# Performance work log

Measured on AMD Instinct MI355X. Metric: run time of the kernel, lower is better.

Reference implementation:

```python
import jax, jax.numpy as jnp
import numpy as np
import math

B, S, D, H = 2, 2048, 1024, 16
DK = D // H


def setup_inputs() -> dict:
    key = jax.random.key(0)
    ks = jax.random.split(key, 14)
    inp = {
        "query": jax.random.normal(ks[0], (B, S, D), dtype=jnp.float32),
        "key": jax.random.normal(ks[1], (B, S, D), dtype=jnp.float32),
        "value": jax.random.normal(ks[2], (B, S, D), dtype=jnp.float32),
        "group_prob": jax.random.uniform(ks[3], (B, S, S), dtype=jnp.float32),
        "mask": jax.random.randint(ks[4], (B, S), 0, 2, dtype=jnp.int32),
    }
    scale = 0.02
    inp["Wq"] = jax.random.normal(ks[5], (D, D), dtype=jnp.float32) * scale
    inp["bq"] = jnp.zeros((D,), dtype=jnp.float32)
    inp["Wk"] = jax.random.normal(ks[6], (D, D), dtype=jnp.float32) * scale
    inp["bk"] = jnp.zeros((D,), dtype=jnp.float32)
    inp["Wv"] = jax.random.normal(ks[7], (D, D), dtype=jnp.float32) * scale
    inp["bv"] = jnp.zeros((D,), dtype=jnp.float32)
    inp["Wo"] = jax.random.normal(ks[8], (D, D), dtype=jnp.float32) * scale
    inp["bo"] = jnp.zeros((D,), dtype=jnp.float32)
    return inp


def reference(query, key, value, group_prob, mask, Wq, bq, Wk, bk, Wv, bv, Wo, bo):
    b, s, d = query.shape
    # project and split heads: [B,S,D] -> [B,H,S,DK]
    def proj(x, W, bias):
        return (x @ W.T + bias).reshape(b, s, H, DK).transpose(0, 2, 1, 3)

    q = proj(query, Wq, bq)
    k = proj(key, Wk, bk)
    v = proj(value, Wv, bv)

    scores = jnp.einsum("bhqd,bhkd->bhqk", q, k) / math.sqrt(DK)  # [B,H,S,S]

    # combined mask: padding-row mask OR diagonal (always attend to self)
    eye = jnp.eye(s, dtype=jnp.int32)
    combined = mask[:, None, None, :] | eye[None, None, :, :]  # [B,1,S,S]
    scores = jnp.where(combined == 0, jnp.float32(-1e9), scores)

    p_attn = jax.nn.softmax(scores, axis=-1)
    p_attn = p_attn * group_prob[:, None, :, :]  # post-softmax group scaling

    x = jnp.einsum("bhqk,bhkd->bhqd", p_attn, v)  # [B,H,S,DK]
    x = x.transpose(0, 2, 1, 3).reshape(b, s, d)
    return x @ Wo.T + bo
```

## Files before the change

### kernel.cpp

```cpp
#include <hip/hip_runtime.h>
#include <hip/hip_bf16.h>
#include <stdint.h>

typedef __bf16 bf16x8 __attribute__((ext_vector_type(8)));
typedef float f32x4 __attribute__((ext_vector_type(4)));

#define QSCALE 0.1803368801111244f

__device__ __forceinline__ void gld16(const void* g, void* l) {
  __builtin_amdgcn_global_load_lds(
      (__attribute__((address_space(1))) void*)(uintptr_t)(g),
      (__attribute__((address_space(3))) void*)(l), 16, 0, 0);
}

struct CastArgs {
  const float* src[7];
  __bf16* dst[7];
  int n[7];
};

__global__ __launch_bounds__(256) void cast_bf16_kernel(CastArgs a) {
  const int t = blockIdx.y;
  const int i = (blockIdx.x * 256 + threadIdx.x) * 8;
  if (i >= a.n[t]) return;
  const float4* s = (const float4*)(a.src[t] + i);
  float4 v0 = s[0], v1 = s[1];
  bf16x8 o;
  o[0] = (__bf16)v0.x; o[1] = (__bf16)v0.y; o[2] = (__bf16)v0.z; o[3] = (__bf16)v0.w;
  o[4] = (__bf16)v1.x; o[5] = (__bf16)v1.y; o[6] = (__bf16)v1.z; o[7] = (__bf16)v1.w;
  *(bf16x8*)(a.dst[t] + i) = o;
}

struct QkvArgs {
  const __bf16* A[3];
  const __bf16* B[3];
  const float* bias[3];
  __bf16* out[3];
};

__global__ __launch_bounds__(256) void qkv_gemm(QkvArgs args) {
  __shared__ __align__(16) __bf16 As[128 * 32];
  __shared__ __align__(16) __bf16 Bs[128 * 32];
  const int tid = threadIdx.x;
  const int z = blockIdx.y;
  const int bx = blockIdx.x;
  const int m0 = (z < 2 ? (bx >> 3) : (bx & 7)) * 128;
  const int n0 = (z < 2 ? (bx & 7) : (bx >> 3)) * 128;
  const __bf16* A = args.A[z];
  const __bf16* B = args.B[z];
  const float* bias = args.bias[z];
  __bf16* out = args.out[z];
  const float scale = (z == 0) ? QSCALE : 1.0f;

  const int lane = tid & 63, wid = tid >> 6;
  const int wm = (wid & 1) * 64, wn = (wid >> 1) * 64;
  const int l16 = lane & 15, quad = lane >> 4;

  const int sc = (tid & 3) ^ ((tid >> 2) & 3);
  const __bf16* ga = A + (size_t)(m0 + (tid >> 2)) * 1024 + sc * 8;
  const __bf16* gb = B + (size_t)(n0 + (tid >> 2)) * 1024 + sc * 8;
  char* lA = (char*)As + tid * 16;
  char* lB = (char*)Bs + tid * 16;
  const int a_off = (wm + l16) * 64 + ((quad ^ (l16 & 3)) * 16);
  const int b_off = (wn + l16) * 64 + ((quad ^ (l16 & 3)) * 16);

  f32x4 acc[4][4] = {};

  for (int k0 = 0; k0 < 1024; k0 += 32) {
    __syncthreads();
    gld16(ga + k0, lA);
    gld16(ga + k0 + 64 * 1024, lA + 4096);
    gld16(gb + k0, lB);
    gld16(gb + k0 + 64 * 1024, lB + 4096);
    __syncthreads();
    bf16x8 af[4], bfr[4];
#pragma unroll
    for (int mi = 0; mi < 4; ++mi)
      af[mi] = *(const bf16x8*)((const char*)As + a_off + mi * 1024);
#pragma unroll
    for (int ni = 0; ni < 4; ++ni)
      bfr[ni] = *(const bf16x8*)((const char*)Bs + b_off + ni * 1024);
#pragma unroll
    for (int mi = 0; mi < 4; ++mi)
#pragma unroll
      for (int ni = 0; ni < 4; ++ni)
        acc[mi][ni] = __builtin_amdgcn_mfma_f32_16x16x32_bf16(af[mi], bfr[ni],
                                                              acc[mi][ni], 0, 0, 0);
  }

  if (z < 2) {
#pragma unroll
    for (int ni = 0; ni < 4; ++ni) {
      const int col = n0 + wn + ni * 16 + l16;
      const int h = col >> 6, dk = col & 63;
      const float bb = bias[col];
#pragma unroll
      for (int mi = 0; mi < 4; ++mi)
#pragma unroll
        for (int r = 0; r < 4; ++r) {
          const int row = m0 + wm + mi * 16 + quad * 4 + r;
          const int b = row >> 11, s = row & 2047;
          out[((size_t)(b * 16 + h) * 2048 + s) * 64 + dk] =
              (__bf16)((acc[mi][ni][r] + bb) * scale);
        }
    }
  } else {
#pragma unroll
    for (int mi = 0; mi < 4; ++mi)
#pragma unroll
      for (int r = 0; r < 4; ++r) {
        const int rowm = m0 + wm + mi * 16 + quad * 4 + r;
        const int h = rowm >> 6, dk = rowm & 63;
        const float bb = bias[rowm];
#pragma unroll
        for (int ni = 0; ni < 4; ++ni) {
          const int coln = n0 + wn + ni * 16 + l16;
          const int b = coln >> 11, s = coln & 2047;
          out[((size_t)(b * 16 + h) * 64 + dk) * 2048 + s] =
              (__bf16)(acc[mi][ni][r] + bb);
        }
      }
  }
}

__global__ __launch_bounds__(256) void gemm_out(const __bf16* __restrict__ A,
                                                const __bf16* __restrict__ B,
                                                const float* __restrict__ bias,
                                                float* __restrict__ out) {
  __shared__ __align__(16) __bf16 As[128 * 32];
  __shared__ __align__(16) __bf16 Bs[128 * 32];
  const int tid = threadIdx.x;
  const int m0 = blockIdx.y * 128;
  const int n0 = blockIdx.x * 128;
  const int lane = tid & 63, wid = tid >> 6;
  const int wm = (wid & 1) * 64, wn = (wid >> 1) * 64;
  const int l16 = lane & 15, quad = lane >> 4;

  const int sc = (tid & 3) ^ ((tid >> 2) & 3);
  const __bf16* ga = A + (size_t)(m0 + (tid >> 2)) * 1024 + sc * 8;
  const __bf16* gb = B + (size_t)(n0 + (tid >> 2)) * 1024 + sc * 8;
  char* lA = (char*)As + tid * 16;
  char* lB = (char*)Bs + tid * 16;
  const int a_off = (wm + l16) * 64 + ((quad ^ (l16 & 3)) * 16);
  const int b_off = (wn + l16) * 64 + ((quad ^ (l16 & 3)) * 16);

  f32x4 acc[4][4] = {};

  for (int k0 = 0; k0 < 1024; k0 += 32) {
    __syncthreads();
    gld16(ga + k0, lA);
    gld16(ga + k0 + 64 * 1024, lA + 4096);
    gld16(gb + k0, lB);
    gld16(gb + k0 + 64 * 1024, lB + 4096);
    __syncthreads();
    bf16x8 af[4], bfr[4];
#pragma unroll
    for (int mi = 0; mi < 4; ++mi)
      af[mi] = *(const bf16x8*)((const char*)As + a_off + mi * 1024);
#pragma unroll
    for (int ni = 0; ni < 4; ++ni)
      bfr[ni] = *(const bf16x8*)((const char*)Bs + b_off + ni * 1024);
#pragma unroll
    for (int mi = 0; mi < 4; ++mi)
#pragma unroll
      for (int ni = 0; ni < 4; ++ni)
        acc[mi][ni] = __builtin_amdgcn_mfma_f32_16x16x32_bf16(af[mi], bfr[ni],
                                                              acc[mi][ni], 0, 0, 0);
  }

#pragma unroll
  for (int ni = 0; ni < 4; ++ni) {
    const int col = n0 + wn + ni * 16 + l16;
    const float bb = bias[col];
#pragma unroll
    for (int mi = 0; mi < 4; ++mi)
#pragma unroll
      for (int r = 0; r < 4; ++r) {
        const int row = m0 + wm + mi * 16 + quad * 4 + r;
        out[(size_t)row * 1024 + col] = acc[mi][ni][r] + bb;
      }
  }
}

__global__ __launch_bounds__(512, 4) void attn_kernel(
    const __bf16* __restrict__ Qh, const __bf16* __restrict__ Kh,
    const __bf16* __restrict__ Vt, const float* __restrict__ gprob,
    const int* __restrict__ maskp, __bf16* __restrict__ xb) {
  __shared__ __align__(16) __bf16 Ks[2][64 * 64];
  __shared__ __align__(16) __bf16 Vs[2][64 * 64];
  __shared__ unsigned long long mbits[32];

  const int tid = threadIdx.x;
  const int qt = blockIdx.x, bh = blockIdx.y;
  const int b = bh >> 4, h = bh & 15;
  const int q0 = qt * 128;
  const int lane = tid & 63, wid = tid >> 6, l16 = lane & 15, quad = lane >> 4;
  const size_t head_off = (size_t)bh * (2048 * 64);

  const int srow = tid >> 3;
  const int sc8 = (tid & 7) ^ (srow & 7);
  const int fxor = (l16 & 7);

  const int sig = ((srow & 16) << 1) + ((srow & 12) << 1) + ((srow & 32) >> 3) +
                  (srow & 3);

  const __bf16* gk0 = Kh + head_off + (size_t)sig * 64 + sc8 * 8;
  const __bf16* gv0 = Vt + head_off + (size_t)srow * 2048 + sc8 * 8;

  gld16(gk0, (char*)Ks + tid * 16);
  gld16(gv0, (char*)Vs + tid * 16);

  bf16x8 aq[2];
  {
    const __bf16* gq = Qh + head_off + (size_t)(q0 + wid * 16 + l16) * 64 + quad * 8;
    aq[0] = *(const bf16x8*)(gq);
    aq[1] = *(const bf16x8*)(gq + 32);
  }

  int irow[4];
#pragma unroll
  for (int r = 0; r < 4; ++r) irow[r] = q0 + wid * 16 + quad * 4 + r;

  const float* gpl = gprob + (size_t)b * 2048 * 2048 +
                     (size_t)(q0 + wid * 16 + l16) * 2048 + quad * 8;
  float4 g0 = *(const float4*)(gpl);
  float4 g1 = *(const float4*)(gpl + 4);
  float4 g2 = *(const float4*)(gpl + 32);
  float4 g3 = *(const float4*)(gpl + 36);

  {
    const int* mr = maskp + b * 2048;
#pragma unroll
    for (int t = 0; t < 4; ++t) {
      const int kt2 = wid * 4 + t;
      const int mv = mr[kt2 * 64 + lane];
      const unsigned long long bal = __ballot(mv != 0);
      if (lane == 0) mbits[kt2] = bal;
    }
  }
  __syncthreads();

  f32x4 o[4] = {};
  float lp = 0.f;

  const int dkt = qt * 2 + (wid >> 2);
  const int kqbase = (wid & 3) * 16 + l16 - quad * 8;

  for (int kt = 0; kt < 32; ++kt) {
    const int cur = kt & 1;
    float4 gn0, gn1, gn2, gn3;
    if (kt < 31) {
      const int nb = cur ^ 1;
      gld16(gk0 + (kt + 1) * 4096, (char*)Ks + nb * 8192 + tid * 16);
      gld16(gv0 + (kt + 1) * 64, (char*)Vs + nb * 8192 + tid * 16);
      const float* gn = gpl + (kt + 1) * 64;
      gn0 = *(const float4*)(gn);
      gn1 = *(const float4*)(gn + 4);
      gn2 = *(const float4*)(gn + 32);
      gn3 = *(const float4*)(gn + 36);
    }

    const unsigned long long sh = mbits[kt] >> (quad * 8);
    const uint32_t shlo = (uint32_t)sh, shhi = (uint32_t)(sh >> 32);

    f32x4 p2[4] = {};
#pragma unroll
    for (int kh = 0; kh < 2; ++kh)
#pragma unroll
      for (int ni = 0; ni < 4; ++ni) {
        bf16x8 bk = *(const bf16x8*)((const char*)Ks + cur * 8192 +
                                     (ni * 16 + l16) * 128 +
                                     (((kh * 4 + quad) ^ fxor) * 16));
        p2[ni] = __builtin_amdgcn_mfma_f32_16x16x32_bf16(bk, aq[kh], p2[ni], 0, 0, 0);
      }

    const float gfl[16] = {g0.x, g0.y, g0.z, g0.w, g1.x, g1.y, g1.z, g1.w,
                           g2.x, g2.y, g2.z, g2.w, g3.x, g3.y, g3.z, g3.w};
    bf16x8 pa0, pa1;
    if (kt != dkt) {
#pragma unroll
      for (int ni = 0; ni < 4; ++ni)
#pragma unroll
        for (int r = 0; r < 4; ++r) {
          const int j = ((ni >> 1) << 2) + r;
          const float e = __builtin_exp2f(p2[ni][r]);
          const bool mk = (((ni & 1) ? shhi : shlo) >> j) & 1;
          const float em = mk ? e : 0.f;
          lp += em;
          const float pg = em * gfl[(ni & 1) * 8 + j];
          if (ni & 1) pa1[j] = (__bf16)pg; else pa0[j] = (__bf16)pg;
        }
    } else {
#pragma unroll
      for (int ni = 0; ni < 4; ++ni)
#pragma unroll
        for (int r = 0; r < 4; ++r) {
          const int j = ((ni >> 1) << 2) + r;
          const float e = __builtin_exp2f(p2[ni][r]);
          const bool mk = (((ni & 1) ? shhi : shlo) >> j) & 1;
          const bool diag = (kqbase == ((ni & 1) * 32 + j));
          const float em = (mk || diag) ? e : 0.f;
          lp += em;
          const float pg = em * gfl[(ni & 1) * 8 + j];
          if (ni & 1) pa1[j] = (__bf16)pg; else pa0[j] = (__bf16)pg;
        }
    }

#pragma unroll
    for (int kh = 0; kh < 2; ++kh) {
      const bf16x8 pa = kh ? pa1 : pa0;
#pragma unroll
      for (int ni = 0; ni < 4; ++ni) {
        bf16x8 bv = *(const bf16x8*)((const char*)Vs + cur * 8192 +
                                     (ni * 16 + l16) * 128 +
                                     (((kh * 4 + quad) ^ fxor) * 16));
        o[ni] = __builtin_amdgcn_mfma_f32_16x16x32_bf16(pa, bv, o[ni], 0, 0, 0);
      }
    }

    if (kt < 31) { g0 = gn0; g1 = gn1; g2 = gn2; g3 = gn3; }
    __syncthreads();
  }

  lp += __shfl_xor(lp, 16);
  lp += __shfl_xor(lp, 32);
  float rinv[4];
#pragma unroll
  for (int r = 0; r < 4; ++r) rinv[r] = 1.f / __shfl(lp, quad * 4 + r);
#pragma unroll
  for (int ni = 0; ni < 4; ++ni) {
    const int dk = ni * 16 + l16;
#pragma unroll
    for (int r = 0; r < 4; ++r) {
      const float val = o[ni][r] * rinv[r];
      xb[((size_t)(b * 2048 + irow[r])) * 1024 + h * 64 + dk] = (__bf16)val;
    }
  }
}

extern "C" void kernel_launch(void* const* d_in, const int* in_sizes, int n_in,
                              void* d_out, int out_size, void* d_ws, size_t ws_size,
                              hipStream_t stream) {
  const float* query = (const float*)d_in[0];
  const float* key_  = (const float*)d_in[1];
  const float* value = (const float*)d_in[2];
  const float* gprob = (const float*)d_in[3];
  const int*   maskp = (const int*)d_in[4];
  const float* Wq = (const float*)d_in[5];
  const float* bq = (const float*)d_in[6];
  const float* Wk = (const float*)d_in[7];
  const float* bk = (const float*)d_in[8];
  const float* Wv = (const float*)d_in[9];
  const float* bv = (const float*)d_in[10];
  const float* Wo = (const float*)d_in[11];
  const float* bo = (const float*)d_in[12];

  char* ws = (char*)d_ws;
  const size_t MB = 1 << 20;
  __bf16* qb  = (__bf16*)(ws + 0 * MB);
  __bf16* kb  = (__bf16*)(ws + 8 * MB);
  __bf16* vb  = (__bf16*)(ws + 16 * MB);
  __bf16* Wqb = (__bf16*)(ws + 24 * MB);
  __bf16* Wkb = (__bf16*)(ws + 26 * MB);
  __bf16* Wvb = (__bf16*)(ws + 28 * MB);
  __bf16* Wob = (__bf16*)(ws + 30 * MB);
  __bf16* Qh  = (__bf16*)(ws + 32 * MB);
  __bf16* Kh  = (__bf16*)(ws + 40 * MB);
  __bf16* Vt  = (__bf16*)(ws + 48 * MB);
  __bf16* xb  = (__bf16*)(ws + 56 * MB);

  CastArgs ca;
  ca.src[0] = query; ca.dst[0] = qb;  ca.n[0] = 4194304;
  ca.src[1] = key_;  ca.dst[1] = kb;  ca.n[1] = 4194304;
  ca.src[2] = value; ca.dst[2] = vb;  ca.n[2] = 4194304;
  ca.src[3] = Wq;    ca.dst[3] = Wqb; ca.n[3] = 1048576;
  ca.src[4] = Wk;    ca.dst[4] = Wkb; ca.n[4] = 1048576;
  ca.src[5] = Wv;    ca.dst[5] = Wvb; ca.n[5] = 1048576;
  ca.src[6] = Wo;    ca.dst[6] = Wob; ca.n[6] = 1048576;
  cast_bf16_kernel<<<dim3(2048, 7), 256, 0, stream>>>(ca);

  QkvArgs qa;
  qa.A[0] = qb;  qa.B[0] = Wqb; qa.bias[0] = bq; qa.out[0] = Qh;
  qa.A[1] = kb;  qa.B[1] = Wkb; qa.bias[1] = bk; qa.out[1] = Kh;
  qa.A[2] = Wvb; qa.B[2] = vb;  qa.bias[2] = bv; qa.out[2] = Vt;
  qkv_gemm<<<dim3(256, 3), 256, 0, stream>>>(qa);

  attn_kernel<<<dim3(16, 32), 512, 0, stream>>>(Qh, Kh, Vt, gprob, maskp, xb);
  gemm_out<<<dim3(8, 32), 256, 0, stream>>>(xb, Wob, bo, (float*)d_out);
}
```

Measured before the change: 301.9 us.

## Process two key tiles per iteration and interleave softmax with MFMA under priority

The attention loop now handles two 64-key tiles per iteration with a double-buffered 128-key LDS stage, halving the number of block barriers. The QK MFMAs for both tiles are issued together and the softmax of tile B is scheduled after tile A's PV MFMAs, with s_setprio raised around the MFMA blocks so matrix work and exp/pack work from different waves overlap. Group-probability loads are issued just in time per tile. LDS use doubles (64KB per block), which may reduce occupancy relative to the declared 4 blocks per CU, and register pressure rises.

```diff
diff --git a/kernel.cpp b/kernel.cpp
--- a/kernel.cpp
+++ b/kernel.cpp
@@ -182,12 +182,33 @@
   }
 }
 
+template <bool DIAG>
+__device__ __forceinline__ void smpack(const f32x4 (&p2)[4], uint32_t shlo,
+                                       uint32_t shhi, const float* gfl,
+                                       int kqbase, float& lp, bf16x8& pa0,
+                                       bf16x8& pa1) {
+#pragma unroll
+  for (int ni = 0; ni < 4; ++ni)
+#pragma unroll
+    for (int r = 0; r < 4; ++r) {
+      const int j = ((ni >> 1) << 2) + r;
+      const float e = __builtin_exp2f(p2[ni][r]);
+      const bool mk = (((ni & 1) ? shhi : shlo) >> j) & 1;
+      bool keep = mk;
+      if (DIAG) keep = mk || (kqbase == ((ni & 1) * 32 + j));
+      const float em = keep ? e : 0.f;
+      lp += em;
+      const float pg = em * gfl[(ni & 1) * 8 + j];
+      if (ni & 1) pa1[j] = (__bf16)pg; else pa0[j] = (__bf16)pg;
+    }
+}
+
 __global__ __launch_bounds__(512, 4) void attn_kernel(
     const __bf16* __restrict__ Qh, const __bf16* __restrict__ Kh,
     const __bf16* __restrict__ Vt, const float* __restrict__ gprob,
     const int* __restrict__ maskp, __bf16* __restrict__ xb) {
-  __shared__ __align__(16) __bf16 Ks[2][64 * 64];
-  __shared__ __align__(16) __bf16 Vs[2][64 * 64];
+  __shared__ __align__(16) __bf16 Ks[2][128 * 64];
+  __shared__ __align__(16) __bf16 Vs[2][128 * 64];
   __shared__ unsigned long long mbits[32];
 
   const int tid = threadIdx.x;
@@ -208,7 +229,9 @@
   const __bf16* gv0 = Vt + head_off + (size_t)srow * 2048 + sc8 * 8;
 
   gld16(gk0, (char*)Ks + tid * 16);
+  gld16(gk0 + 4096, (char*)Ks + 8192 + tid * 16);
   gld16(gv0, (char*)Vs + tid * 16);
+  gld16(gv0 + 64, (char*)Vs + 8192 + tid * 16);
 
   bf16x8 aq[2];
   {
@@ -217,16 +240,12 @@
     aq[1] = *(const bf16x8*)(gq + 32);
   }
 
-  int irow[4];
-#pragma unroll
-  for (int r = 0; r < 4; ++r) irow[r] = q0 + wid * 16 + quad * 4 + r;
-
   const float* gpl = gprob + (size_t)b * 2048 * 2048 +
                      (size_t)(q0 + wid * 16 + l16) * 2048 + quad * 8;
-  float4 g0 = *(const float4*)(gpl);
-  float4 g1 = *(const float4*)(gpl + 4);
-  float4 g2 = *(const float4*)(gpl + 32);
-  float4 g3 = *(const float4*)(gpl + 36);
+  float4 gA0 = *(const float4*)(gpl);
+  float4 gA1 = *(const float4*)(gpl + 4);
+  float4 gA2 = *(const float4*)(gpl + 32);
+  float4 gA3 = *(const float4*)(gpl + 36);
 
   {
     const int* mr = maskp + b * 2048;
@@ -246,79 +265,103 @@
   const int dkt = qt * 2 + (wid >> 2);
   const int kqbase = (wid & 3) * 16 + l16 - quad * 8;
 
-  for (int kt = 0; kt < 32; ++kt) {
-    const int cur = kt & 1;
-    float4 gn0, gn1, gn2, gn3;
-    if (kt < 31) {
+  for (int tt = 0; tt < 16; ++tt) {
+    const int cur = tt & 1;
+    const int kkA = 2 * tt, kkB = 2 * tt + 1;
+    if (tt < 15) {
       const int nb = cur ^ 1;
-      gld16(gk0 + (kt + 1) * 4096, (char*)Ks + nb * 8192 + tid * 16);
-      gld16(gv0 + (kt + 1) * 64, (char*)Vs + nb * 8192 + tid * 16);
-      const float* gn = gpl + (kt + 1) * 64;
-      gn0 = *(const float4*)(gn);
-      gn1 = *(const float4*)(gn + 4);
-      gn2 = *(const float4*)(gn + 32);
-      gn3 = *(const float4*)(gn + 36);
-    }
-
-    const unsigned long long sh = mbits[kt] >> (quad * 8);
-    const uint32_t shlo = (uint32_t)sh, shhi = (uint32_t)(sh >> 32);
-
-    f32x4 p2[4] = {};
+      gld16(gk0 + (size_t)(kkA + 2) * 4096, (char*)Ks + nb * 16384 + tid * 16);
+      gld16(gk0 + (size_t)(kkB + 2) * 4096, (char*)Ks + nb * 16384 + 8192 + tid * 16);
+      gld16(gv0 + (kkA + 2) * 64, (char*)Vs + nb * 16384 + tid * 16);
+      gld16(gv0 + (kkB + 2) * 64, (char*)Vs + nb * 16384 + 8192 + tid * 16);
+    }
+    const float* gbp = gpl + (size_t)kkB * 64;
+    float4 gB0 = *(const float4*)(gbp);
+    float4 gB1 = *(const float4*)(gbp + 4);
+    float4 gB2 = *(const float4*)(gbp + 32);
+    float4 gB3 = *(const float4*)(gbp + 36);
+
+    const unsigned long long shA = mbits[kkA] >> (quad * 8);
+    const unsigned long long shB = mbits[kkB] >> (quad * 8);
+
+    f32x4 p2a[4] = {}, p2b[4] = {};
+    const char* ksA = (const char*)Ks + cur * 16384;
+    const char* ksB = ksA + 8192;
+    __builtin_amdgcn_s_setprio(1);
 #pragma unroll
     for (int kh = 0; kh < 2; ++kh)
 #pragma unroll
       for (int ni = 0; ni < 4; ++ni) {
-        bf16x8 bk = *(const bf16x8*)((const char*)Ks + cur * 8192 +
-                                     (ni * 16 + l16) * 128 +
+        bf16x8 bk = *(const bf16x8*)(ksA + (ni * 16 + l16) * 128 +
                                      (((kh * 4 + quad) ^ fxor) * 16));
-        p2[ni] = __builtin_amdgcn_mfma_f32_16x16x32_bf16(bk, aq[kh], p2[ni], 0, 0, 0);
-      }
-
-    const float gfl[16] = {g0.x, g0.y, g0.z, g0.w, g1.x, g1.y, g1.z, g1.w,
-                           g2.x, g2.y, g2.z, g2.w, g3.x, g3.y, g3.z, g3.w};
-    bf16x8 pa0, pa1;
-    if (kt != dkt) {
-#pragma unroll
-      for (int ni = 0; ni < 4; ++ni)
-#pragma unroll
-        for (int r = 0; r < 4; ++r) {
-          const int j = ((ni >> 1) << 2) + r;
-          const float e = __builtin_exp2f(p2[ni][r]);
-          const bool mk = (((ni & 1) ? shhi : shlo) >> j) & 1;
-          const float em = mk ? e : 0.f;
-          lp += em;
-          const float pg = em * gfl[(ni & 1) * 8 + j];
-          if (ni & 1) pa1[j] = (__bf16)pg; else pa0[j] = (__bf16)pg;
-        }
-    } else {
-#pragma unroll
-      for (int ni = 0; ni < 4; ++ni)
-#pragma unroll
-        for (int r = 0; r < 4; ++r) {
-          const int j = ((ni >> 1) << 2) + r;
-          const float e = __builtin_exp2f(p2[ni][r]);
-          const bool mk = (((ni & 1) ? shhi : shlo) >> j) & 1;
-          const bool diag = (kqbase == ((ni & 1) * 32 + j));
-          const float em = (mk || diag) ? e : 0.f;
-          lp += em;
-          const float pg = em * gfl[(ni & 1) * 8 + j];
-          if (ni & 1) pa1[j] = (__bf16)pg; else pa0[j] = (__bf16)pg;
-        }
-    }
-
+        p2a[ni] = __builtin_amdgcn_mfma_f32_16x16x32_bf16(bk, aq[kh], p2a[ni], 0, 0, 0);
+      }
+#pragma unroll
+    for (int kh = 0; kh < 2; ++kh)
+#pragma unroll
+      for (int ni = 0; ni < 4; ++ni) {
+        bf16x8 bk = *(const bf16x8*)(ksB + (ni * 16 + l16) * 128 +
+                                     (((kh * 4 + quad) ^ fxor) * 16));
+        p2b[ni] = __builtin_amdgcn_mfma_f32_16x16x32_bf16(bk, aq[kh], p2b[ni], 0, 0, 0);
+      }
+    __builtin_amdgcn_s_setprio(0);
+
+    bf16x8 paA0, paA1;
+    {
+      const float gfl[16] = {gA0.x, gA0.y, gA0.z, gA0.w, gA1.x, gA1.y, gA1.z, gA1.w,
+                             gA2.x, gA2.y, gA2.z, gA2.w, gA3.x, gA3.y, gA3.z, gA3.w};
+      if (kkA == dkt)
+        smpack<true>(p2a, (uint32_t)shA, (uint32_t)(shA >> 32), gfl, kqbase, lp, paA0, paA1);
+      else
+        smpack<false>(p2a, (uint32_t)shA, (uint32_t)(shA >> 32), gfl, kqbase, lp, paA0, paA1);
+    }
+
+    const char* vsA = (const char*)Vs + cur * 16384;
+    const char* vsB = vsA + 8192;
+    __builtin_amdgcn_s_setprio(1);
 #pragma unroll
     for (int kh = 0; kh < 2; ++kh) {
-      const bf16x8 pa = kh ? pa1 : pa0;
+      const bf16x8 pa = kh ? paA1 : paA0;
 #pragma unroll
       for (int ni = 0; ni < 4; ++ni) {
-        bf16x8 bv = *(const bf16x8*)((const char*)Vs + cur * 8192 +
-                                     (ni * 16 + l16) * 128 +
+        bf16x8 bv = *(const bf16x8*)(vsA + (ni * 16 + l16) * 128 +
                                      (((kh * 4 + quad) ^ fxor) * 16));
         o[ni] = __builtin_amdgcn_mfma_f32_16x16x32_bf16(pa, bv, o[ni], 0, 0, 0);
       }
     }
-
-    if (kt < 31) { g0 = gn0; g1 = gn1; g2 = gn2; g3 = gn3; }
+    __builtin_amdgcn_s_setprio(0);
+
+    if (tt < 15) {
+      const float* gap = gpl + (size_t)(kkA + 2) * 64;
+      gA0 = *(const float4*)(gap);
+      gA1 = *(const float4*)(gap + 4);
+      gA2 = *(const float4*)(gap + 32);
+      gA3 = *(const float4*)(gap + 36);
+    }
+
+    bf16x8 paB0, paB1;
+    {
+      const float gfl[16] = {gB0.x, gB0.y, gB0.z, gB0.w, gB1.x, gB1.y, gB1.z, gB1.w,
+                             gB2.x, gB2.y, gB2.z, gB2.w, gB3.x, gB3.y, gB3.z, gB3.w};
+      if (kkB == dkt)
+        smpack<true>(p2b, (uint32_t)shB, (uint32_t)(shB >> 32), gfl, kqbase, lp, paB0, paB1);
+      else
+        smpack<false>(p2b, (uint32_t)shB, (uint32_t)(shB >> 32), gfl, kqbase, lp, paB0, paB1);
+    }
+
+    __builtin_amdgcn_s_setprio(1);
+#pragma unroll
+    for (int kh = 0; kh < 2; ++kh) {
+      const bf16x8 pa = kh ? paB1 : paB0;
+#pragma unroll
+      for (int ni = 0; ni < 4; ++ni) {
+        bf16x8 bv = *(const bf16x8*)(vsB + (ni * 16 + l16) * 128 +
+                                     (((kh * 4 + quad) ^ fxor) * 16));
+        o[ni] = __builtin_amdgcn_mfma_f32_16x16x32_bf16(pa, bv, o[ni], 0, 0, 0);
+      }
+    }
+    __builtin_amdgcn_s_setprio(0);
+
     __syncthreads();
   }
 
@@ -327,6 +370,9 @@
   float rinv[4];
 #pragma unroll
   for (int r = 0; r < 4; ++r) rinv[r] = 1.f / __shfl(lp, quad * 4 + r);
+  int irow[4];
+#pragma unroll
+  for (int r = 0; r < 4; ++r) irow[r] = q0 + wid * 16 + quad * 4 + r;
 #pragma unroll
   for (int ni = 0; ni < 4; ++ni) {
     const int dk = ni * 16 + l16;
```

Result: slower. 318.5 us (+5.5%).
